# Performance work log

Measured on AMD Instinct MI355X. Metric: run time of the kernel, lower is better.

## Reference

```python
import jax, jax.numpy as jnp
import numpy as np

EPS = 1e-6
TEMP_GEO = 0.07
W_LOCAL = 0.5
W_SHARP = 0.5


def _l2norm(x):
    return x / jnp.clip(jnp.linalg.norm(x, axis=-1, keepdims=True), 1e-12)


def setup_inputs() -> dict:
    key = jax.random.key(0)
    ks = jax.random.split(key, 6)
    B, L, S, C = 8, 1024, 1024, 128
    N, P = 8, 256
    q_geo = _l2norm(jax.random.normal(ks[0], (B, L, C), jnp.float32))
    geo_pos = _l2norm(jax.random.normal(ks[1], (B, S, C), jnp.float32))
    label = jax.random.randint(ks[2], (B, L, S), 0, 2, jnp.int32)
    q_cl = jax.random.normal(ks[3], (N, P, C), jnp.float32)
    cl_pos = jax.random.normal(ks[4], (N, P, C), jnp.float32)
    idx = jax.random.randint(ks[5], (N,), 0, P, jnp.int32)
    return {"q_geo": q_geo, "q_cl": q_cl, "geo_pos": geo_pos,
            "cl_pos": cl_pos, "label": label, "idx": idx}


def _masked_mean(v, m):
    # per-sample mean over the [L,S] plane of entries where m is True
    m = m.astype(v.dtype)
    return jnp.sum(v * m, axis=(1, 2)) / jnp.maximum(jnp.sum(m, axis=(1, 2)), 1.0)


def _loftr_loss(conf, label):
    # standard LoFTR coarse CE loss (LoFTRLoss source absent from repo snippet)
    conf = jnp.clip(conf, EPS, 1.0 - EPS)
    pos = label == 1
    neg = label == 0
    pos_loss = _masked_mean(-jnp.log(conf), pos)          # [B]
    neg_loss = _masked_mean(-jnp.log(1.0 - conf), neg)    # [B]
    loss = pos_loss + neg_loss
    return jnp.mean(loss), jnp.mean(pos_loss), jnp.mean(neg_loss)


def _geometric_loss(q, k, label):
    sim = jnp.einsum('blc,bsc->bls', q, k) / TEMP_GEO        # [B,L,S]
    conf = jax.nn.softmax(sim, axis=1) * jax.nn.softmax(sim, axis=2)
    return _loftr_loss(conf, label)


def _sharpness_loss(q, k, label):
    sim = (1.0 + jnp.einsum('blc,bsc->bls', q, k)) / 2.0     # [B,L,S]
    # column stats (over L, dim=0 per sample) -> sharpness1 [B,S]
    s1 = (jnp.max(sim, axis=1) - jnp.mean(sim, axis=1)) / jnp.std(sim, axis=1, ddof=1)
    sharp1 = jax.nn.softmax(s1, axis=-1)
    # row stats (over S, dim=1 per sample) -> sharpness2 [B,L]
    s2 = (jnp.max(sim, axis=2) - jnp.mean(sim, axis=2)) / jnp.std(sim, axis=2, ddof=1)
    sharp2 = jax.nn.softmax(s2, axis=-1)
    simc = jnp.clip(sim, EPS, 1.0 - EPS)
    nll = -jnp.log(simc)
    pos = (label == 1).astype(simc.dtype)
    neg = (label == 0)
    loss1 = jnp.sum(nll * sharp1[:, None, :] * pos, axis=(1, 2))   # [B]
    loss2 = jnp.sum(nll * sharp2[:, :, None] * pos, axis=(1, 2))   # [B]
    loss3 = _masked_mean(-jnp.log(1.0 - simc), neg)                # [B]
    losses = (loss1 + loss2) / 2.0 + loss3
    return sharp1, jnp.mean(losses)


def _contrast_loss(q, all_k):
    # intended math of GeCoContrast: full cosine matrix, diag positives, tail negatives
    N = q.shape[0]
    sim = (1.0 + _l2norm(q) @ _l2norm(all_k).T) / 2.0   # [N, M]
    sim = jnp.clip(sim, EPS, 1.0 - EPS)
    l_pos = jnp.diagonal(sim[:, :N])                    # [N]
    l_neg = sim[:, N:]                                  # [N, M-N]
    return (jnp.mean(-jnp.log(l_pos)) + jnp.mean(-jnp.log(1.0 - l_neg))) / 2.0


def _forward(q_geo, q_cl, geo_pos, cl_pos, label, idx):
    loss_geo, geo_pos_loss, geo_neg_loss = _geometric_loss(q_geo, geo_pos, label)
    sharpness, loss_sharp = _sharpness_loss(q_geo, geo_pos, label)
    loss_geo = ((1.0 - W_SHARP) * loss_geo + W_SHARP * loss_sharp) * W_LOCAL

    N, P, C = q_cl.shape
    ar = jnp.arange(N)
    q_sel = q_cl[ar, idx]                               # [N,C]
    sel = cl_pos[ar, idx]                               # [N,C] positives moved to slot 0
    first = cl_pos[:, 0, :]
    swapped = cl_pos.at[ar, idx].set(first).at[:, 0, :].set(sel)
    cl_pos_save = sel
    all_k = jnp.concatenate([swapped[:, 0, :],
                             swapped[:, 1:, :].reshape(N * (P - 1), C)], axis=0)
    loss_cl = _contrast_loss(q_sel, all_k) * (1.0 - W_LOCAL)

    total = loss_geo + loss_cl
    return (sharpness, cl_pos_save, total, geo_pos_loss, geo_neg_loss, loss_sharp, loss_cl)


def reference(q_geo, q_cl, geo_pos, cl_pos, label, idx):
    return _forward(q_geo, q_cl, geo_pos, cl_pos, label, idx)
```

## Files before the change

kernel.cpp:

```cpp
#include <hip/hip_runtime.h>
#include <math.h>

#define BB 8
#define LL 1024
#define SS 1024
#define CC 128
#define NN 8
#define PP 256

static constexpr float EPS       = 1e-6f;
static constexpr float ONE_M_EPS = 1.0f - 1e-6f;
static constexpr float INV_T     = 1.0f / 0.07f;
static constexpr float NLL_MAX   = 13.815511f;
static constexpr float NLL_MIN   = 1.0000005e-6f;

static constexpr size_t DOTSZ      = (size_t)BB * LL * SS;
static constexpr size_t OFF_LSER   = DOTSZ;
static constexpr size_t OFF_S2RAW  = DOTSZ + 8192;
static constexpr size_t OFF_LSEC   = DOTSZ + 16384;
static constexpr size_t OFF_S1RAW  = DOTSZ + 24576;
static constexpr size_t OFF_SHARP2 = DOTSZ + 32768;
static constexpr size_t OFF_RP     = DOTSZ + 40960;
static constexpr size_t OFF_CP     = OFF_RP + 524288;
static constexpr size_t OFF_ACC    = OFF_CP + 524288;
static constexpr size_t OFF_ACCCL  = OFF_ACC + 48;
static constexpr size_t OFF_QN     = OFF_ACC + 64;

static constexpr int OUT_CLSAVE = 8192;
static constexpr int OUT_SCAL   = 9216;

typedef __bf16 bf16x8 __attribute__((ext_vector_type(8)));
typedef float  floatx4 __attribute__((ext_vector_type(4)));

__device__ __forceinline__ bf16x8 mkfrag(unsigned a, unsigned b, unsigned c, unsigned d) {
    uint4 t = make_uint4(a, b, c, d);
    return __builtin_bit_cast(bf16x8, t);
}

__device__ __forceinline__ void split_f4(float4 x,
                                         unsigned& hp0, unsigned& hp1,
                                         unsigned& lp0, unsigned& lp1) {
    unsigned u0 = __builtin_bit_cast(unsigned, x.x);
    unsigned u1 = __builtin_bit_cast(unsigned, x.y);
    unsigned u2 = __builtin_bit_cast(unsigned, x.z);
    unsigned u3 = __builtin_bit_cast(unsigned, x.w);
    unsigned r0 = u0 + 0x7FFFu + ((u0 >> 16) & 1u);
    unsigned r1 = u1 + 0x7FFFu + ((u1 >> 16) & 1u);
    unsigned r2 = u2 + 0x7FFFu + ((u2 >> 16) & 1u);
    unsigned r3 = u3 + 0x7FFFu + ((u3 >> 16) & 1u);
    float s0 = x.x - __builtin_bit_cast(float, r0 & 0xFFFF0000u);
    float s1 = x.y - __builtin_bit_cast(float, r1 & 0xFFFF0000u);
    float s2 = x.z - __builtin_bit_cast(float, r2 & 0xFFFF0000u);
    float s3 = x.w - __builtin_bit_cast(float, r3 & 0xFFFF0000u);
    hp0 = __builtin_amdgcn_perm(r1, r0, 0x07060302u);
    hp1 = __builtin_amdgcn_perm(r3, r2, 0x07060302u);
    lp0 = __builtin_amdgcn_perm(__builtin_bit_cast(unsigned, s1),
                                __builtin_bit_cast(unsigned, s0), 0x07060302u);
    lp1 = __builtin_amdgcn_perm(__builtin_bit_cast(unsigned, s3),
                                __builtin_bit_cast(unsigned, s2), 0x07060302u);
}

__global__ __launch_bounds__(512) void prep(const float* __restrict__ q_cl,
                                            const float* __restrict__ cl_pos,
                                            const int* __restrict__ idx,
                                            float* __restrict__ out, float* __restrict__ ws) {
    int tid = threadIdx.x;
    if (tid < 50) ws[OFF_ACC + tid] = 0.0f;
    int n = tid >> 6, lane = tid & 63;
    int in = idx[n];
    const float* q = q_cl + ((size_t)(n * PP + in)) * CC;
    float2 qv = *(const float2*)(q + 2 * lane);
    float ss = qv.x * qv.x + qv.y * qv.y;
    for (int o = 32; o; o >>= 1) ss += __shfl_xor(ss, o);
    float inv = 1.0f / fmaxf(sqrtf(ss), 1e-12f);
    *(float2*)(ws + OFF_QN + n * 128 + 2 * lane) = make_float2(qv.x * inv, qv.y * inv);
    const float* cp = cl_pos + ((size_t)(n * PP + in)) * CC;
    float2 cv = *(const float2*)(cp + 2 * lane);
    *(float2*)(out + OUT_CLSAVE + n * 128 + 2 * lane) = cv;
}

__global__ __launch_bounds__(256) void gemm_dot(const float* __restrict__ A,
                                                const float* __restrict__ Bm,
                                                float* __restrict__ dot,
                                                float* __restrict__ ws) {
    int tid  = threadIdx.x;
    int lane = tid & 63;
    int w    = tid >> 6;
    int t    = blockIdx.x * 4 + w;
    int b    = t >> 8;
    int rem  = t & 255;
    int lt   = rem >> 4, st = rem & 15;
    int l0   = lt * 64, s0 = st * 64;
    int fl   = lane & 15;
    int quad = lane >> 4;

    const float* Ab = A  + ((size_t)b * LL + l0) * CC;
    const float* Bb = Bm + ((size_t)b * SS + s0) * CC;

    floatx4 acc[4][4];
#pragma unroll
    for (int i = 0; i < 4; i++)
#pragma unroll
        for (int j = 0; j < 4; j++) acc[i][j] = (floatx4){0.f, 0.f, 0.f, 0.f};

    for (int c0 = 0; c0 < 128; c0 += 32) {
        float4 ax[4][2], bx[4][2];
#pragma unroll
        for (int mt = 0; mt < 4; mt++) {
            const float* p = Ab + (size_t)(mt * 16 + fl) * CC + c0 + quad * 8;
            ax[mt][0] = *(const float4*)p;
            ax[mt][1] = *(const float4*)(p + 4);
        }
#pragma unroll
        for (int nt = 0; nt < 4; nt++) {
            const float* p = Bb + (size_t)(nt * 16 + fl) * CC + c0 + quad * 8;
            bx[nt][0] = *(const float4*)p;
            bx[nt][1] = *(const float4*)(p + 4);
        }
        bf16x8 ah[4], al[4];
#pragma unroll
        for (int mt = 0; mt < 4; mt++) {
            unsigned h0, h1, h2, h3, q0, q1, q2, q3;
            split_f4(ax[mt][0], h0, h1, q0, q1);
            split_f4(ax[mt][1], h2, h3, q2, q3);
            ah[mt] = mkfrag(h0, h1, h2, h3);
            al[mt] = mkfrag(q0, q1, q2, q3);
        }
#pragma unroll
        for (int nt = 0; nt < 4; nt++) {
            unsigned h0, h1, h2, h3, q0, q1, q2, q3;
            split_f4(bx[nt][0], h0, h1, q0, q1);
            split_f4(bx[nt][1], h2, h3, q2, q3);
            bf16x8 bh = mkfrag(h0, h1, h2, h3);
            bf16x8 bl = mkfrag(q0, q1, q2, q3);
#pragma unroll
            for (int mt = 0; mt < 4; mt++) {
                acc[mt][nt] = __builtin_amdgcn_mfma_f32_16x16x32_bf16(ah[mt], bh, acc[mt][nt], 0, 0, 0);
                acc[mt][nt] = __builtin_amdgcn_mfma_f32_16x16x32_bf16(ah[mt], bl, acc[mt][nt], 0, 0, 0);
                acc[mt][nt] = __builtin_amdgcn_mfma_f32_16x16x32_bf16(al[mt], bh, acc[mt][nt], 0, 0, 0);
            }
        }
    }

    float* D = dot + ((size_t)b * LL + l0) * SS + s0;
#pragma unroll
    for (int mt = 0; mt < 4; mt++)
#pragma unroll
        for (int nt = 0; nt < 4; nt++) {
            int col = nt * 16 + fl;
#pragma unroll
            for (int r = 0; r < 4; r++) {
                int row = mt * 16 + quad * 4 + r;
                D[(size_t)row * SS + col] = acc[mt][nt][r];
            }
        }

    float ces[4], cmx[4], csm[4], csq[4];
#pragma unroll
    for (int nt = 0; nt < 4; nt++) { ces[nt] = 0.f; cmx[nt] = -1e30f; csm[nt] = 0.f; csq[nt] = 0.f; }
#pragma unroll
    for (int mt = 0; mt < 4; mt++) {
#pragma unroll
        for (int r = 0; r < 4; r++) {
            float es = 0.f, mx = -1e30f, sm = 0.f, sq = 0.f;
#pragma unroll
            for (int nt = 0; nt < 4; nt++) {
                float d  = acc[mt][nt][r];
                float e  = __expf(d * INV_T);
                float s2 = fmaf(0.5f, d, 0.5f);
                es += e; mx = fmaxf(mx, s2); sm += s2; sq += s2 * s2;
                ces[nt] += e; cmx[nt] = fmaxf(cmx[nt], s2); csm[nt] += s2; csq[nt] += s2 * s2;
            }
            for (int o = 1; o < 16; o <<= 1) {
                es += __shfl_xor(es, o);
                mx = fmaxf(mx, __shfl_xor(mx, o));
                sm += __shfl_xor(sm, o);
                sq += __shfl_xor(sq, o);
            }
            if (fl == 0) {
                int row = l0 + mt * 16 + quad * 4 + r;
                *(float4*)(ws + OFF_RP + (((size_t)(b * 16 + st)) * 1024 + row) * 4) =
                    make_float4(es, mx, sm, sq);
            }
        }
    }
#pragma unroll
    for (int nt = 0; nt < 4; nt++) {
        float es = ces[nt], mx = cmx[nt], sm = csm[nt], sq = csq[nt];
        for (int o = 16; o < 64; o <<= 1) {
            es += __shfl_xor(es, o);
            mx = fmaxf(mx, __shfl_xor(mx, o));
            sm += __shfl_xor(sm, o);
            sq += __shfl_xor(sq, o);
        }
        if (quad == 0) {
            int col = s0 + nt * 16 + fl;
            *(float4*)(ws + OFF_CP + (((size_t)(b * 16 + lt)) * 1024 + col) * 4) =
                make_float4(es, mx, sm, sq);
        }
    }
}

__global__ __launch_bounds__(256) void rc_combine(float* __restrict__ ws) {
    int g = (blockIdx.x & 31) * 256 + threadIdx.x;
    bool docol = blockIdx.x >= 32;
    int b = g >> 10, i = g & 1023;
    const float* part = ws + (docol ? OFF_CP : OFF_RP);
    float es = 0.f, mx = -1e30f, sm = 0.f, sq = 0.f;
#pragma unroll
    for (int t = 0; t < 16; t++) {
        float4 v = *(const float4*)(part + (((size_t)(b * 16 + t)) * 1024 + i) * 4);
        es += v.x; mx = fmaxf(mx, v.y); sm += v.z; sq += v.w;
    }
    float mean = sm * (1.0f / 1024.0f);
    float var  = (sq - sm * sm * (1.0f / 1024.0f)) * (1.0f / 1023.0f);
    float zs   = (mx - mean) / sqrtf(fmaxf(var, 1e-30f));
    if (!docol) {
        ws[OFF_LSER + g]  = __logf(es);
        ws[OFF_S2RAW + g] = zs;
    } else {
        ws[OFF_LSEC + g]  = __logf(es);
        ws[OFF_S1RAW + g] = zs;
    }
}

__global__ __launch_bounds__(256) void softmax16(float* __restrict__ ws, float* __restrict__ out) {
    int q = blockIdx.x;
    int b = q & 7;
    const float* src = ws + ((q < 8) ? OFF_S1RAW : OFF_S2RAW) + (size_t)b * 1024;
    float* dst = (q < 8) ? (out + (size_t)b * 1024) : (ws + OFF_SHARP2 + (size_t)b * 1024);
    float4 v = ((const float4*)src)[threadIdx.x];
    int lane = threadIdx.x & 63, wid = threadIdx.x >> 6;
    __shared__ float sb[4];
    __shared__ float red;
    float mx = fmaxf(fmaxf(v.x, v.y), fmaxf(v.z, v.w));
    for (int o = 32; o; o >>= 1) mx = fmaxf(mx, __shfl_xor(mx, o));
    if (!lane) sb[wid] = mx;
    __syncthreads();
    if (threadIdx.x == 0) red = fmaxf(fmaxf(sb[0], sb[1]), fmaxf(sb[2], sb[3]));
    __syncthreads();
    mx = red;
    float e0 = __expf(v.x - mx), e1 = __expf(v.y - mx), e2 = __expf(v.z - mx), e3 = __expf(v.w - mx);
    float sm = e0 + e1 + e2 + e3;
    for (int o = 32; o; o >>= 1) sm += __shfl_xor(sm, o);
    __syncthreads();
    if (!lane) sb[wid] = sm;
    __syncthreads();
    if (threadIdx.x == 0) red = sb[0] + sb[1] + sb[2] + sb[3];
    __syncthreads();
    float inv = 1.0f / red;
    ((float4*)dst)[threadIdx.x] = make_float4(e0 * inv, e1 * inv, e2 * inv, e3 * inv);
}

__device__ __forceinline__ void proc_elem(float d, int lab, float lcj, float sh1j,
                                          float lr, float s2v,
                                          float& posg, float& negg, float& l1, float& l2,
                                          float& negs, float& pcf) {
    float t = lr + lcj - d * (2.0f * INV_T);
    float isPos = (lab == 1) ? 1.0f : 0.0f;
    float isNeg = 1.0f - isPos;
    float tp   = fminf(fmaxf(t, NLL_MIN), NLL_MAX);
    float simc = fminf(fmaxf(fmaf(0.5f, d, 0.5f), EPS), ONE_M_EPS);
    float om   = fminf(fmaxf(fmaf(-0.5f, d, 0.5f), EPS), ONE_M_EPS);
    float nll2 = -__logf(simc);
    float cf   = fminf(fmaxf(__expf(-t), EPS), ONE_M_EPS);
    float nllg = -__logf(1.0f - cf);
    float nlls = -__logf(om);
    posg += isPos * tp;
    l1   += isPos * nll2 * sh1j;
    l2   += isPos * nll2 * s2v;
    pcf  += isPos;
    negg += isNeg * nllg;
    negs += isNeg * nlls;
}

__global__ __launch_bounds__(256) void main_loss(const float* __restrict__ dot,
                                                 const int* __restrict__ label,
                                                 const float* __restrict__ sharp1,
                                                 float* __restrict__ ws) {
    int b = blockIdx.y;
    int l0 = blockIdx.x * 4;
    int s = threadIdx.x * 4;
    float4 lc4 = *(const float4*)(ws + OFF_LSEC + (size_t)b * 1024 + s);
    float4 sh1 = *(const float4*)(sharp1 + (size_t)b * 1024 + s);
    const float* lser = ws + OFF_LSER + (size_t)b * 1024;
    const float* sh2  = ws + OFF_SHARP2 + (size_t)b * 1024;
    float posg = 0, negg = 0, l1 = 0, l2 = 0, negs = 0, pcf = 0;
#pragma unroll
    for (int r = 0; r < 4; r++) {
        int l = l0 + r;
        float lr  = lser[l];
        float s2v = sh2[l];
        size_t base = ((size_t)(b * 1024 + l)) * 1024 + s;
        float4 d4 = *(const float4*)(dot + base);
        int4  lb  = *(const int4*)(label + base);
        proc_elem(d4.x, lb.x, lc4.x, sh1.x, lr, s2v, posg, negg, l1, l2, negs, pcf);
        proc_elem(d4.y, lb.y, lc4.y, sh1.y, lr, s2v, posg, negg, l1, l2, negs, pcf);
        proc_elem(d4.z, lb.z, lc4.z, sh1.z, lr, s2v, posg, negg, l1, l2, negs, pcf);
        proc_elem(d4.w, lb.w, lc4.w, sh1.w, lr, s2v, posg, negg, l1, l2, negs, pcf);
    }
    float vals[6] = {posg, negg, l1, l2, negs, pcf};
    __shared__ float sb[6][4];
    int lane = threadIdx.x & 63, wid = threadIdx.x >> 6;
#pragma unroll
    for (int k = 0; k < 6; k++) {
        float v = vals[k];
        for (int o = 32; o; o >>= 1) v += __shfl_xor(v, o);
        if (!lane) sb[k][wid] = v;
    }
    __syncthreads();
    if (threadIdx.x < 6) {
        float r = sb[threadIdx.x][0] + sb[threadIdx.x][1] + sb[threadIdx.x][2] + sb[threadIdx.x][3];
        atomicAdd(ws + OFF_ACC + (size_t)b * 6 + threadIdx.x, r);
    }
}

__global__ __launch_bounds__(256) void contrast(const float* __restrict__ cl_pos,
                                                const int* __restrict__ idx,
                                                float* __restrict__ ws) {
    int j = blockIdx.x * 4 + (threadIdx.x >> 6);
    int lane = threadIdx.x & 63;
    int m, p;
    if (j < NN) {
        m = j; p = idx[j];
    } else {
        int jj = j - NN;
        m = jj / (PP - 1);
        p = 1 + (jj - m * (PP - 1));
        if (p == idx[m]) p = 0;
    }
    const float* k = cl_pos + ((size_t)(m * PP + p)) * CC;
    float2 kv = *(const float2*)(k + 2 * lane);
    float ksq = kv.x * kv.x + kv.y * kv.y;
    for (int o = 32; o; o >>= 1) ksq += __shfl_xor(ksq, o);
    float invkn = 1.0f / fmaxf(sqrtf(ksq), 1e-12f);
    float pos = 0.0f, neg = 0.0f;
    if (j < NN) {
        const float2 qv = *(const float2*)(ws + OFF_QN + j * 128 + 2 * lane);
        float dt = qv.x * kv.x + qv.y * kv.y;
        for (int o = 32; o; o >>= 1) dt += __shfl_xor(dt, o);
        float sim = fminf(fmaxf(fmaf(0.5f * invkn, dt, 0.5f), EPS), ONE_M_EPS);
        pos = -__logf(sim);
    } else {
#pragma unroll
        for (int n = 0; n < NN; n++) {
            const float2 qv = *(const float2*)(ws + OFF_QN + n * 128 + 2 * lane);
            float dt = qv.x * kv.x + qv.y * kv.y;
            for (int o = 32; o; o >>= 1) dt += __shfl_xor(dt, o);
            float om = fminf(fmaxf(fmaf(-0.5f * invkn, dt, 0.5f), EPS), ONE_M_EPS);
            neg -= __logf(om);
        }
    }
    __shared__ float sb[2][4];
    int w = threadIdx.x >> 6;
    if (!lane) { sb[0][w] = pos; sb[1][w] = neg; }
    __syncthreads();
    if (threadIdx.x == 0) {
        float ps = sb[0][0] + sb[0][1] + sb[0][2] + sb[0][3];
        float ng = sb[1][0] + sb[1][1] + sb[1][2] + sb[1][3];
        if (ps != 0.0f) atomicAdd(ws + OFF_ACCCL + 0, ps);
        if (ng != 0.0f) atomicAdd(ws + OFF_ACCCL + 1, ng);
    }
}

__global__ void finalize(float* __restrict__ out, const float* __restrict__ ws) {
    if (threadIdx.x != 0) return;
    float gp = 0, gn = 0, lsh = 0;
    for (int b = 0; b < 8; b++) {
        const float* a = ws + OFF_ACC + (size_t)b * 6;
        float pc = a[5];
        float nc = (float)((size_t)LL * SS) - pc;
        gp += a[0] / fmaxf(pc, 1.0f);
        gn += a[1] / fmaxf(nc, 1.0f);
        lsh += (a[2] + a[3]) * 0.5f + a[4] / fmaxf(nc, 1.0f);
    }
    gp *= 0.125f; gn *= 0.125f; lsh *= 0.125f;
    float lgeo = gp + gn;
    float lgw = (0.5f * lgeo + 0.5f * lsh) * 0.5f;
    float clp = ws[OFF_ACCCL + 0] / 8.0f;
    float cln = ws[OFF_ACCCL + 1] / (8.0f * 2040.0f);
    float lcl = (clp + cln) * 0.5f * 0.5f;
    out[OUT_SCAL + 0] = lgw + lcl;
    out[OUT_SCAL + 1] = gp;
    out[OUT_SCAL + 2] = gn;
    out[OUT_SCAL + 3] = lsh;
    out[OUT_SCAL + 4] = lcl;
}

extern "C" void kernel_launch(void* const* d_in, const int* in_sizes, int n_in,
                              void* d_out, int out_size, void* d_ws, size_t ws_size,
                              hipStream_t stream) {
    const float* q_geo   = (const float*)d_in[0];
    const float* q_cl    = (const float*)d_in[1];
    const float* geo_pos = (const float*)d_in[2];
    const float* cl_pos  = (const float*)d_in[3];
    const int*   label   = (const int*)d_in[4];
    const int*   idx     = (const int*)d_in[5];
    float* out = (float*)d_out;
    float* ws  = (float*)d_ws;
    float* dot = ws;

    prep<<<dim3(1), dim3(512), 0, stream>>>(q_cl, cl_pos, idx, out, ws);
    gemm_dot<<<dim3(512), dim3(256), 0, stream>>>(q_geo, geo_pos, dot, ws);
    rc_combine<<<dim3(64), dim3(256), 0, stream>>>(ws);
    softmax16<<<dim3(16), dim3(256), 0, stream>>>(ws, out);
    main_loss<<<dim3(256, 8), dim3(256), 0, stream>>>(dot, label, out, ws);
    contrast<<<dim3(512), dim3(256), 0, stream>>>(cl_pos, idx, ws);
    finalize<<<dim3(1), dim3(64), 0, stream>>>(out, ws);
}
```

Baseline: 163.7 us.

## Pre-split inputs to bf16 hi/lo, LDS-tiled GEMM, separate stats pass

Adds a conversion kernel that splits both fp32 inputs into bf16 hi/lo parts once, laid out as a 384-wide K axis so the three-term product becomes a single GEMM. The GEMM now uses 128x128 block tiles staged through shared memory with direct global-to-LDS loads, instead of each wave reloading and re-splitting fp32 data from global memory. The fused row/column statistics epilogue moves into a separate stats kernel that rereads the 32 MB dot matrix, plus a column-combine kernel. This trades redundant splitting and global loads for an extra full read of the dot matrix and more launches.

```diff
diff --git a/kernel.cpp b/kernel.cpp
--- a/kernel.cpp
+++ b/kernel.cpp
@@ -20,11 +20,12 @@
 static constexpr size_t OFF_LSEC   = DOTSZ + 16384;
 static constexpr size_t OFF_S1RAW  = DOTSZ + 24576;
 static constexpr size_t OFF_SHARP2 = DOTSZ + 32768;
-static constexpr size_t OFF_RP     = DOTSZ + 40960;
-static constexpr size_t OFF_CP     = OFF_RP + 524288;
-static constexpr size_t OFF_ACC    = OFF_CP + 524288;
+static constexpr size_t OFF_CP     = DOTSZ + 40960;
+static constexpr size_t OFF_ACC    = OFF_CP + 2097152;
 static constexpr size_t OFF_ACCCL  = OFF_ACC + 48;
 static constexpr size_t OFF_QN     = OFF_ACC + 64;
+static constexpr size_t OFF_AH     = OFF_ACC + 2048;
+static constexpr size_t OFF_BH     = OFF_AH + 1572864;
 
 static constexpr int OUT_CLSAVE = 8192;
 static constexpr int OUT_SCAL   = 9216;
@@ -32,32 +33,22 @@
 typedef __bf16 bf16x8 __attribute__((ext_vector_type(8)));
 typedef float  floatx4 __attribute__((ext_vector_type(4)));
 
-__device__ __forceinline__ bf16x8 mkfrag(unsigned a, unsigned b, unsigned c, unsigned d) {
-    uint4 t = make_uint4(a, b, c, d);
-    return __builtin_bit_cast(bf16x8, t);
-}
-
-__device__ __forceinline__ void split_f4(float4 x,
-                                         unsigned& hp0, unsigned& hp1,
-                                         unsigned& lp0, unsigned& lp1) {
+__device__ __forceinline__ void gld_lds16(const void* g, void* l) {
+    __builtin_amdgcn_global_load_lds(
+        (const __attribute__((address_space(1))) void*)g,
+        (__attribute__((address_space(3))) void*)l, 16, 0, 0);
+}
+
+__device__ __forceinline__ void split2(float2 x, unsigned& hp, unsigned& lp) {
     unsigned u0 = __builtin_bit_cast(unsigned, x.x);
     unsigned u1 = __builtin_bit_cast(unsigned, x.y);
-    unsigned u2 = __builtin_bit_cast(unsigned, x.z);
-    unsigned u3 = __builtin_bit_cast(unsigned, x.w);
     unsigned r0 = u0 + 0x7FFFu + ((u0 >> 16) & 1u);
     unsigned r1 = u1 + 0x7FFFu + ((u1 >> 16) & 1u);
-    unsigned r2 = u2 + 0x7FFFu + ((u2 >> 16) & 1u);
-    unsigned r3 = u3 + 0x7FFFu + ((u3 >> 16) & 1u);
     float s0 = x.x - __builtin_bit_cast(float, r0 & 0xFFFF0000u);
     float s1 = x.y - __builtin_bit_cast(float, r1 & 0xFFFF0000u);
-    float s2 = x.z - __builtin_bit_cast(float, r2 & 0xFFFF0000u);
-    float s3 = x.w - __builtin_bit_cast(float, r3 & 0xFFFF0000u);
-    hp0 = __builtin_amdgcn_perm(r1, r0, 0x07060302u);
-    hp1 = __builtin_amdgcn_perm(r3, r2, 0x07060302u);
-    lp0 = __builtin_amdgcn_perm(__builtin_bit_cast(unsigned, s1),
-                                __builtin_bit_cast(unsigned, s0), 0x07060302u);
-    lp1 = __builtin_amdgcn_perm(__builtin_bit_cast(unsigned, s3),
-                                __builtin_bit_cast(unsigned, s2), 0x07060302u);
+    hp = __builtin_amdgcn_perm(r1, r0, 0x07060302u);
+    lp = __builtin_amdgcn_perm(__builtin_bit_cast(unsigned, s1),
+                               __builtin_bit_cast(unsigned, s0), 0x07060302u);
 }
 
 __global__ __launch_bounds__(512) void prep(const float* __restrict__ q_cl,
@@ -79,23 +70,41 @@
     *(float2*)(out + OUT_CLSAVE + n * 128 + 2 * lane) = cv;
 }
 
-__global__ __launch_bounds__(256) void gemm_dot(const float* __restrict__ A,
-                                                const float* __restrict__ Bm,
-                                                float* __restrict__ dot,
-                                                float* __restrict__ ws) {
+__global__ __launch_bounds__(256) void convert(const float* __restrict__ q_geo,
+                                               const float* __restrict__ geo_pos,
+                                               float* __restrict__ ws) {
+    int r = blockIdx.x * 4 + (threadIdx.x >> 6);
+    int lane = threadIdx.x & 63;
+    bool isB = r >= 8192;
+    int rr = isB ? r - 8192 : r;
+    const float* src = (isB ? geo_pos : q_geo) + (size_t)rr * CC + 2 * lane;
+    short* dst = (short*)(ws + (isB ? OFF_BH : OFF_AH)) + (size_t)rr * 384 + 2 * lane;
+    float2 v = *(const float2*)src;
+    unsigned hp, lp;
+    split2(v, hp, lp);
+    *(unsigned*)(dst + 0)   = hp;
+    *(unsigned*)(dst + 128) = isB ? lp : hp;
+    *(unsigned*)(dst + 256) = isB ? hp : lp;
+}
+
+__global__ __launch_bounds__(256) void gemm_dot(const float* __restrict__ wsc,
+                                                float* __restrict__ dot) {
+    int b  = blockIdx.z;
+    int l0 = blockIdx.y * 128;
+    int s0 = blockIdx.x * 128;
+    __shared__ short As[128 * 32];
+    __shared__ short Bs[128 * 32];
+
     int tid  = threadIdx.x;
     int lane = tid & 63;
     int w    = tid >> 6;
-    int t    = blockIdx.x * 4 + w;
-    int b    = t >> 8;
-    int rem  = t & 255;
-    int lt   = rem >> 4, st = rem & 15;
-    int l0   = lt * 64, s0 = st * 64;
+    int wr   = (w >> 1) * 64;
+    int wc   = (w & 1) * 64;
     int fl   = lane & 15;
     int quad = lane >> 4;
 
-    const float* Ab = A  + ((size_t)b * LL + l0) * CC;
-    const float* Bb = Bm + ((size_t)b * SS + s0) * CC;
+    const short* AH = (const short*)(wsc + OFF_AH) + ((size_t)(b * 1024 + l0)) * 384;
+    const short* BH = (const short*)(wsc + OFF_BH) + ((size_t)(b * 1024 + s0)) * 384;
 
     floatx4 acc[4][4];
 #pragma unroll
@@ -103,125 +112,119 @@
 #pragma unroll
         for (int j = 0; j < 4; j++) acc[i][j] = (floatx4){0.f, 0.f, 0.f, 0.f};
 
-    for (int c0 = 0; c0 < 128; c0 += 32) {
-        float4 ax[4][2], bx[4][2];
-#pragma unroll
-        for (int mt = 0; mt < 4; mt++) {
-            const float* p = Ab + (size_t)(mt * 16 + fl) * CC + c0 + quad * 8;
-            ax[mt][0] = *(const float4*)p;
-            ax[mt][1] = *(const float4*)(p + 4);
-        }
+    for (int kk = 0; kk < 12; kk++) {
+        int k0 = kk * 32;
+#pragma unroll
+        for (int rep = 0; rep < 2; rep++) {
+            int c   = tid + rep * 256;
+            int row = c >> 2;
+            int ko  = (c & 3) * 8;
+            gld_lds16(AH + (size_t)row * 384 + k0 + ko, &As[c * 8]);
+            gld_lds16(BH + (size_t)row * 384 + k0 + ko, &Bs[c * 8]);
+        }
+        __syncthreads();
+
+        bf16x8 af[4], bf[4];
+#pragma unroll
+        for (int mt = 0; mt < 4; mt++)
+            af[mt] = *reinterpret_cast<const bf16x8*>(&As[(wr + mt * 16 + fl) * 32 + quad * 8]);
+#pragma unroll
+        for (int nt = 0; nt < 4; nt++)
+            bf[nt] = *reinterpret_cast<const bf16x8*>(&Bs[(wc + nt * 16 + fl) * 32 + quad * 8]);
+#pragma unroll
+        for (int nt = 0; nt < 4; nt++)
+#pragma unroll
+            for (int mt = 0; mt < 4; mt++)
+                acc[mt][nt] = __builtin_amdgcn_mfma_f32_16x16x32_bf16(af[mt], bf[nt], acc[mt][nt], 0, 0, 0);
+        __syncthreads();
+    }
+
+    float* D = dot + ((size_t)b * LL + l0) * SS + s0;
+#pragma unroll
+    for (int mt = 0; mt < 4; mt++)
 #pragma unroll
         for (int nt = 0; nt < 4; nt++) {
-            const float* p = Bb + (size_t)(nt * 16 + fl) * CC + c0 + quad * 8;
-            bx[nt][0] = *(const float4*)p;
-            bx[nt][1] = *(const float4*)(p + 4);
-        }
-        bf16x8 ah[4], al[4];
-#pragma unroll
-        for (int mt = 0; mt < 4; mt++) {
-            unsigned h0, h1, h2, h3, q0, q1, q2, q3;
-            split_f4(ax[mt][0], h0, h1, q0, q1);
-            split_f4(ax[mt][1], h2, h3, q2, q3);
-            ah[mt] = mkfrag(h0, h1, h2, h3);
-            al[mt] = mkfrag(q0, q1, q2, q3);
-        }
-#pragma unroll
-        for (int nt = 0; nt < 4; nt++) {
-            unsigned h0, h1, h2, h3, q0, q1, q2, q3;
-            split_f4(bx[nt][0], h0, h1, q0, q1);
-            split_f4(bx[nt][1], h2, h3, q2, q3);
-            bf16x8 bh = mkfrag(h0, h1, h2, h3);
-            bf16x8 bl = mkfrag(q0, q1, q2, q3);
-#pragma unroll
-            for (int mt = 0; mt < 4; mt++) {
-                acc[mt][nt] = __builtin_amdgcn_mfma_f32_16x16x32_bf16(ah[mt], bh, acc[mt][nt], 0, 0, 0);
-                acc[mt][nt] = __builtin_amdgcn_mfma_f32_16x16x32_bf16(ah[mt], bl, acc[mt][nt], 0, 0, 0);
-                acc[mt][nt] = __builtin_amdgcn_mfma_f32_16x16x32_bf16(al[mt], bh, acc[mt][nt], 0, 0, 0);
-            }
-        }
-    }
-
-    float* D = dot + ((size_t)b * LL + l0) * SS + s0;
-#pragma unroll
-    for (int mt = 0; mt < 4; mt++)
-#pragma unroll
-        for (int nt = 0; nt < 4; nt++) {
-            int col = nt * 16 + fl;
+            int col = wc + nt * 16 + fl;
 #pragma unroll
             for (int r = 0; r < 4; r++) {
-                int row = mt * 16 + quad * 4 + r;
+                int row = wr + mt * 16 + quad * 4 + r;
                 D[(size_t)row * SS + col] = acc[mt][nt][r];
             }
         }
-
-    float ces[4], cmx[4], csm[4], csq[4];
-#pragma unroll
-    for (int nt = 0; nt < 4; nt++) { ces[nt] = 0.f; cmx[nt] = -1e30f; csm[nt] = 0.f; csq[nt] = 0.f; }
-#pragma unroll
-    for (int mt = 0; mt < 4; mt++) {
-#pragma unroll
-        for (int r = 0; r < 4; r++) {
-            float es = 0.f, mx = -1e30f, sm = 0.f, sq = 0.f;
-#pragma unroll
-            for (int nt = 0; nt < 4; nt++) {
-                float d  = acc[mt][nt][r];
-                float e  = __expf(d * INV_T);
-                float s2 = fmaf(0.5f, d, 0.5f);
-                es += e; mx = fmaxf(mx, s2); sm += s2; sq += s2 * s2;
-                ces[nt] += e; cmx[nt] = fmaxf(cmx[nt], s2); csm[nt] += s2; csq[nt] += s2 * s2;
-            }
-            for (int o = 1; o < 16; o <<= 1) {
-                es += __shfl_xor(es, o);
-                mx = fmaxf(mx, __shfl_xor(mx, o));
-                sm += __shfl_xor(sm, o);
-                sq += __shfl_xor(sq, o);
-            }
-            if (fl == 0) {
-                int row = l0 + mt * 16 + quad * 4 + r;
-                *(float4*)(ws + OFF_RP + (((size_t)(b * 16 + st)) * 1024 + row) * 4) =
-                    make_float4(es, mx, sm, sq);
-            }
-        }
-    }
-#pragma unroll
-    for (int nt = 0; nt < 4; nt++) {
-        float es = ces[nt], mx = cmx[nt], sm = csm[nt], sq = csq[nt];
-        for (int o = 16; o < 64; o <<= 1) {
+}
+
+__global__ __launch_bounds__(256) void stats(const float* __restrict__ dot, float* __restrict__ ws) {
+    int b  = blockIdx.x >> 6;
+    int lc = blockIdx.x & 63;
+    int tid = threadIdx.x;
+    int col0 = tid * 4;
+    float res[16], rmx[16], rsm[16], rsq[16];
+    float ces[4] = {0, 0, 0, 0}, csm[4] = {0, 0, 0, 0}, csq[4] = {0, 0, 0, 0};
+    float cmx[4] = {-1e30f, -1e30f, -1e30f, -1e30f};
+#pragma unroll
+    for (int r = 0; r < 16; r++) {
+        int row = lc * 16 + r;
+        float4 d4 = *(const float4*)(dot + ((size_t)(b * 1024 + row)) * 1024 + col0);
+        float vals[4] = {d4.x, d4.y, d4.z, d4.w};
+        float es = 0.f, mx = -1e30f, sm = 0.f, sq = 0.f;
+#pragma unroll
+        for (int j = 0; j < 4; j++) {
+            float d  = vals[j];
+            float e  = __expf(d * INV_T);
+            float s2 = fmaf(0.5f, d, 0.5f);
+            es += e; mx = fmaxf(mx, s2); sm += s2; sq += s2 * s2;
+            ces[j] += e; cmx[j] = fmaxf(cmx[j], s2); csm[j] += s2; csq[j] += s2 * s2;
+        }
+        res[r] = es; rmx[r] = mx; rsm[r] = sm; rsq[r] = sq;
+    }
+#pragma unroll
+    for (int j = 0; j < 4; j++) {
+        *(float4*)(ws + OFF_CP + (((size_t)(b * 64 + lc)) * 1024 + col0 + j) * 4) =
+            make_float4(ces[j], cmx[j], csm[j], csq[j]);
+    }
+    __shared__ float sred[16][4][4];
+    int lane = tid & 63, wid = tid >> 6;
+#pragma unroll
+    for (int r = 0; r < 16; r++) {
+        float es = res[r], mx = rmx[r], sm = rsm[r], sq = rsq[r];
+        for (int o = 32; o; o >>= 1) {
             es += __shfl_xor(es, o);
             mx = fmaxf(mx, __shfl_xor(mx, o));
             sm += __shfl_xor(sm, o);
             sq += __shfl_xor(sq, o);
         }
-        if (quad == 0) {
-            int col = s0 + nt * 16 + fl;
-            *(float4*)(ws + OFF_CP + (((size_t)(b * 16 + lt)) * 1024 + col) * 4) =
-                make_float4(es, mx, sm, sq);
-        }
-    }
-}
-
-__global__ __launch_bounds__(256) void rc_combine(float* __restrict__ ws) {
-    int g = (blockIdx.x & 31) * 256 + threadIdx.x;
-    bool docol = blockIdx.x >= 32;
-    int b = g >> 10, i = g & 1023;
-    const float* part = ws + (docol ? OFF_CP : OFF_RP);
+        if (!lane) { sred[r][wid][0] = es; sred[r][wid][1] = mx; sred[r][wid][2] = sm; sred[r][wid][3] = sq; }
+    }
+    __syncthreads();
+    if (tid < 16) {
+        float es = 0.f, mx = -1e30f, sm = 0.f, sq = 0.f;
+#pragma unroll
+        for (int w2 = 0; w2 < 4; w2++) {
+            es += sred[tid][w2][0];
+            mx = fmaxf(mx, sred[tid][w2][1]);
+            sm += sred[tid][w2][2];
+            sq += sred[tid][w2][3];
+        }
+        int l = lc * 16 + tid;
+        ws[OFF_LSER + (size_t)b * 1024 + l] = __logf(es);
+        float mean = sm * (1.0f / 1024.0f);
+        float var  = (sq - sm * sm * (1.0f / 1024.0f)) * (1.0f / 1023.0f);
+        ws[OFF_S2RAW + (size_t)b * 1024 + l] = (mx - mean) / sqrtf(fmaxf(var, 1e-30f));
+    }
+}
+
+__global__ __launch_bounds__(256) void ccomb(float* __restrict__ ws) {
+    int g = blockIdx.x * 256 + threadIdx.x;
+    int b = g >> 10, s = g & 1023;
     float es = 0.f, mx = -1e30f, sm = 0.f, sq = 0.f;
-#pragma unroll
-    for (int t = 0; t < 16; t++) {
-        float4 v = *(const float4*)(part + (((size_t)(b * 16 + t)) * 1024 + i) * 4);
+    for (int t = 0; t < 64; t++) {
+        float4 v = *(const float4*)(ws + OFF_CP + (((size_t)(b * 64 + t)) * 1024 + s) * 4);
         es += v.x; mx = fmaxf(mx, v.y); sm += v.z; sq += v.w;
     }
+    ws[OFF_LSEC + g] = __logf(es);
     float mean = sm * (1.0f / 1024.0f);
     float var  = (sq - sm * sm * (1.0f / 1024.0f)) * (1.0f / 1023.0f);
-    float zs   = (mx - mean) / sqrtf(fmaxf(var, 1e-30f));
-    if (!docol) {
-        ws[OFF_LSER + g]  = __logf(es);
-        ws[OFF_S2RAW + g] = zs;
-    } else {
-        ws[OFF_LSEC + g]  = __logf(es);
-        ws[OFF_S1RAW + g] = zs;
-    }
+    ws[OFF_S1RAW + g] = (mx - mean) / sqrtf(fmaxf(var, 1e-30f));
 }
 
 __global__ __launch_bounds__(256) void softmax16(float* __restrict__ ws, float* __restrict__ out) {
@@ -401,8 +404,10 @@
     float* dot = ws;
 
     prep<<<dim3(1), dim3(512), 0, stream>>>(q_cl, cl_pos, idx, out, ws);
-    gemm_dot<<<dim3(512), dim3(256), 0, stream>>>(q_geo, geo_pos, dot, ws);
-    rc_combine<<<dim3(64), dim3(256), 0, stream>>>(ws);
+    convert<<<dim3(4096), dim3(256), 0, stream>>>(q_geo, geo_pos, ws);
+    gemm_dot<<<dim3(8, 8, 8), dim3(256), 0, stream>>>(ws, dot);
+    stats<<<dim3(512), dim3(256), 0, stream>>>(dot, ws);
+    ccomb<<<dim3(32), dim3(256), 0, stream>>>(ws);
     softmax16<<<dim3(16), dim3(256), 0, stream>>>(ws, out);
     main_loss<<<dim3(256, 8), dim3(256), 0, stream>>>(dot, label, out, ws);
     contrast<<<dim3(512), dim3(256), 0, stream>>>(cl_pos, idx, ws);
```

After: 177.1 us. +8.2%, slower.
